# Kernel tuning notes

Hardware: AMD Instinct MI355X
Metric: run time of the kernel (lower is better)

Reference implementation:

```python
import jax, jax.numpy as jnp
import numpy as np
import math

B, S, HID = 2, 2048, 2048
NH, NKV, HD = 16, 4, 128
ROPE_BASE = 10000.0

def _rope(x, position_ids):
    # x: [B, H, S, HD], position_ids: [B, S]
    half = HD // 2
    inv_freq = 1.0 / (ROPE_BASE ** (jnp.arange(0, half, dtype=jnp.float32) / half))
    freqs = position_ids.astype(jnp.float32)[:, :, None] * inv_freq[None, None, :]  # [B,S,half]
    cos = jnp.cos(freqs)[:, None, :, :]  # [B,1,S,half]
    sin = jnp.sin(freqs)[:, None, :, :]
    x1, x2 = x[..., :half], x[..., half:]
    return jnp.concatenate([x1 * cos - x2 * sin, x2 * cos + x1 * sin], axis=-1)

def setup_inputs() -> dict:
    key = jax.random.key(0)
    k1, k2, k3 = jax.random.split(key, 3)
    x = jax.random.normal(k1, (B, S, HID), dtype=jnp.float32)
    position_ids = jnp.broadcast_to(jnp.arange(S, dtype=jnp.int64 if jax.config.jax_enable_x64 else jnp.int32)[None, :], (B, S))
    causal = jnp.tril(jnp.ones((S, S), dtype=bool))
    mask = jnp.where(causal, 0.0, -1e9).astype(jnp.float32)[None, None, :, :]
    w_qkv = jax.random.normal(k2, (NH * HD + 2 * NKV * HD, HID), dtype=jnp.float32) * 0.02
    w_o = jax.random.normal(k3, (HID, HID), dtype=jnp.float32) * 0.02
    return {"x": x, "position_ids": position_ids, "mask": mask, "w_qkv": w_qkv, "w_o": w_o}

def reference(x, position_ids, mask, w_qkv, w_o):
    qkv = x @ w_qkv.T  # [B,S,3072]
    q_dim, kv_dim = NH * HD, NKV * HD
    q = qkv[..., :q_dim].reshape(B, S, NH, HD).transpose(0, 2, 1, 3)          # [B,NH,S,HD]
    k = qkv[..., q_dim:q_dim + kv_dim].reshape(B, S, NKV, HD).transpose(0, 2, 1, 3)
    v = qkv[..., q_dim + kv_dim:].reshape(B, S, NKV, HD).transpose(0, 2, 1, 3)
    q = _rope(q, position_ids)
    k = _rope(k, position_ids)
    n_rep = NH // NKV
    k = jnp.repeat(k, n_rep, axis=1)  # [B,NH,S,HD]
    v = jnp.repeat(v, n_rep, axis=1)
    scores = jnp.einsum('bhqd,bhkd->bhqk', q, k) / math.sqrt(HD) + mask
    attn = jax.nn.softmax(scores, axis=-1)  # dropout p=0.0 -> identity
    out = jnp.einsum('bhqk,bhkd->bhqd', attn, v)
    out = out.transpose(0, 2, 1, 3).reshape(B, S, HID)
    return out @ w_o.T
```

## Files before the change

### kernel.cpp

```cpp
#include <hip/hip_runtime.h>
#include <hip/hip_bf16.h>
#include <cstdint>
#include <cstddef>

typedef unsigned short u16;
typedef __attribute__((ext_vector_type(8))) __bf16 bf16x8;
typedef __attribute__((ext_vector_type(4))) float floatx4;

#define B_    2
#define S_    2048
#define HID_  2048
#define NH_   16
#define NKV_  4
#define HD_   128
#define QKVN_ 3072

__device__ __forceinline__ float bf2f(u16 u) {
  union { unsigned int i; float f; } v; v.i = ((unsigned int)u) << 16; return v.f;
}
__device__ __forceinline__ u16 f2bf(float f) {
  union { float f; unsigned int i; } v; v.f = f;
  unsigned int u = v.i;
  return (u16)((u + 0x7fffu + ((u >> 16) & 1u)) >> 16);
}

#define GLOAD_LDS16(gp, lp)                                                  \
  __builtin_amdgcn_global_load_lds(                                          \
      (__attribute__((address_space(1))) void*)(gp),                         \
      (__attribute__((address_space(3))) void*)(lp), 16, 0, 0)

__global__ __launch_bounds__(256)
void cast_f32_bf16(const float* __restrict__ in, u16* __restrict__ out, int n)
{
  const int i = (blockIdx.x * 256 + threadIdx.x) * 8;
  if (i >= n) return;
  const float4 a = *(const float4*)(in + i);
  const float4 b = *(const float4*)(in + i + 4);
  union { u16 h[8]; uint4 v; } o;
  o.h[0] = f2bf(a.x); o.h[1] = f2bf(a.y); o.h[2] = f2bf(a.z); o.h[3] = f2bf(a.w);
  o.h[4] = f2bf(b.x); o.h[5] = f2bf(b.y); o.h[6] = f2bf(b.z); o.h[7] = f2bf(b.w);
  *(uint4*)(out + i) = o.v;
}

template <bool F32OUT>
__global__ __launch_bounds__(256, 2)
void gemm_bt_128(const u16* __restrict__ A, const u16* __restrict__ W,
                 void* __restrict__ Cv, int N, int K, int lda, int ldc)
{
  __shared__ __align__(16) u16 lA[128 * 64];
  __shared__ __align__(16) u16 lB[128 * 64];
  const int tid  = threadIdx.x;
  const int w    = tid >> 6, ln = tid & 63;
  const int quad = ln >> 4,  l15 = ln & 15;
  const int m0 = blockIdx.y * 128, n0 = blockIdx.x * 128;
  const int waveM = (w >> 1) * 64, waveN = (w & 1) * 64;

  const floatx4 vzero = {0.f, 0.f, 0.f, 0.f};
  floatx4 acc[4][4];
#pragma unroll
  for (int i = 0; i < 4; ++i)
#pragma unroll
    for (int j = 0; j < 4; ++j) acc[i][j] = vzero;

  for (int k0 = 0; k0 < K; k0 += 64) {
    __syncthreads();
#pragma unroll
    for (int p = 0; p < 4; ++p) {
      const int L = (p * 4 + w) * 64 + ln;
      const int row = L >> 3, c = L & 7;
      GLOAD_LDS16(A + (size_t)(m0 + row) * lda + k0 + c * 8, lA + L * 8);
      GLOAD_LDS16(W + (size_t)(n0 + row) * K   + k0 + c * 8, lB + L * 8);
    }
    __syncthreads();
#pragma unroll
    for (int kk = 0; kk < 64; kk += 32) {
      bf16x8 aF[4], bF[4];
      const int cbase = (kk >> 3) + quad;
#pragma unroll
      for (int t = 0; t < 4; ++t) {
        const int rowA = waveM + t * 16 + l15;
        aF[t] = *(const bf16x8*)(lA + rowA * 64 + cbase * 8);
        const int rowB = waveN + t * 16 + l15;
        bF[t] = *(const bf16x8*)(lB + rowB * 64 + cbase * 8);
      }
#pragma unroll
      for (int i = 0; i < 4; ++i)
#pragma unroll
        for (int j = 0; j < 4; ++j)
          acc[i][j] = __builtin_amdgcn_mfma_f32_16x16x32_bf16(aF[i], bF[j], acc[i][j], 0, 0, 0);
    }
  }
#pragma unroll
  for (int i = 0; i < 4; ++i)
#pragma unroll
    for (int r = 0; r < 4; ++r) {
      const int row = m0 + waveM + i * 16 + quad * 4 + r;
      if (F32OUT) {
        float* cp = (float*)Cv + (size_t)row * ldc + n0 + waveN + l15;
#pragma unroll
        for (int j = 0; j < 4; ++j) cp[j * 16] = acc[i][j][r];
      } else {
        u16* cp = (u16*)Cv + (size_t)row * ldc + n0 + waveN + l15;
#pragma unroll
        for (int j = 0; j < 4; ++j) cp[j * 16] = f2bf(acc[i][j][r]);
      }
    }
}

__global__ __launch_bounds__(256)
void rope_inplace(u16* __restrict__ qkv, u16* __restrict__ vt_ws)
{
  const int s = blockIdx.x, b = blockIdx.y;
  const int tid = threadIdx.x;
  __shared__ float cs[64], sn[64];
  if (tid < 64) {
    const float inv = powf(10000.0f, -((float)tid) / 64.0f);
    float s_, c_;
    sincosf((float)s * inv, &s_, &c_);
    cs[tid] = c_; sn[tid] = s_;
  }
  __syncthreads();
  u16* base = qkv + ((size_t)b * S_ + s) * QKVN_;
  for (int p = tid; p < NH_ * 64; p += 256) {
    const int h = p >> 6, i = p & 63;
    u16* hp = base + h * 128;
    const float x1 = bf2f(hp[i]);
    const float x2 = bf2f(hp[64 + i]);
    hp[i]      = f2bf(x1 * cs[i] - x2 * sn[i]);
    hp[64 + i] = f2bf(x2 * cs[i] + x1 * sn[i]);
  }
  for (int p = tid; p < NKV_ * 64; p += 256) {
    const int h = p >> 6, i = p & 63;
    u16* hp = base + NH_ * HD_ + h * 128;
    const float x1 = bf2f(hp[i]);
    const float x2 = bf2f(hp[64 + i]);
    hp[i]      = f2bf(x1 * cs[i] - x2 * sn[i]);
    hp[64 + i] = f2bf(x2 * cs[i] + x1 * sn[i]);
  }
  for (int p = tid; p < NKV_ * HD_; p += 256) {
    const int h = p >> 7, d = p & 127;
    vt_ws[((size_t)(b * NKV_ + h) * HD_ + d) * S_ + s] =
        base[NH_ * HD_ + NKV_ * HD_ + h * 128 + d];
  }
}

#define LPP 68
#define KSLOT(key, s) ((key) * 128 + (((s) ^ ((key) & 7)) * 8))
#define VSLOT(d, s)   ((d) * 64  + (((s) ^ ((d) & 7)) * 8))

__global__ __launch_bounds__(256, 2)
void flash_attn(u16* __restrict__ qkv, const u16* __restrict__ vt_ws)
{
  const int qt = 31 - (int)blockIdx.x;
  const int h  = blockIdx.y;
  const int b  = blockIdx.z;
  const int tid  = threadIdx.x;
  const int w    = tid >> 6, ln = tid & 63;
  const int quad = ln >> 4,  l15 = ln & 15;
  const int kvh  = h >> 2;

  __shared__ __align__(16) u16 lK[2][64 * 128];
  __shared__ __align__(16) u16 lVt[2][128 * 64];
  __shared__ __align__(16) u16 lP[4][16 * LPP];

  const float scale = 0.08838834764831845f;
  const u16* kbase = qkv + (size_t)b * S_ * QKVN_ + NH_ * HD_ + kvh * HD_;
  const u16* vbase = vt_ws + (size_t)(b * NKV_ + kvh) * HD_ * S_;
  const floatx4 vzero = {0.f, 0.f, 0.f, 0.f};

  const int qrow0 = qt * 64 + w * 16;

  bf16x8 qF[4];
  {
    const u16* qp = qkv + ((size_t)(b * S_) + qrow0 + l15) * QKVN_ + h * HD_;
#pragma unroll
    for (int c = 0; c < 4; ++c)
      qF[c] = *(const bf16x8*)(qp + c * 32 + quad * 8);
  }

  float m_i[4], l_i[4];
  floatx4 Oacc[8];
#pragma unroll
  for (int r = 0; r < 4; ++r) { m_i[r] = -1e30f; l_i[r] = 0.f; }
#pragma unroll
  for (int t = 0; t < 8; ++t) Oacc[t] = vzero;

#pragma unroll
  for (int p = 0; p < 4; ++p) {
    const int idx = (w * 4 + p) * 64 + ln;
    const int key = idx >> 4, ks = idx & 15;
    GLOAD_LDS16(kbase + (size_t)key * QKVN_ + ((ks ^ (key & 7)) * 8),
                lK[0] + (w * 4 + p) * 512);
    const int d = idx >> 3, vs = idx & 7;
    GLOAD_LDS16(vbase + (size_t)d * S_ + ((vs ^ (d & 7)) * 8),
                lVt[0] + (w * 4 + p) * 512);
  }

  const int ktEnd = qt + 1;
#pragma unroll 1
  for (int kt = 0; kt < ktEnd; ++kt) {
    const u16* lKc = lK[kt & 1];
    const u16* lVc = lVt[kt & 1];
    const bool pf = (kt + 1 < ktEnd);
    if (pf) {
      u16* lKn = lK[(kt + 1) & 1];
      u16* lVn = lVt[(kt + 1) & 1];
#pragma unroll
      for (int p = 0; p < 4; ++p) {
        const int idx = (w * 4 + p) * 64 + ln;
        const int key = idx >> 4, ks = idx & 15;
        GLOAD_LDS16(kbase + (size_t)((kt + 1) * 64 + key) * QKVN_ + ((ks ^ (key & 7)) * 8),
                    lKn + (w * 4 + p) * 512);
        const int d = idx >> 3, vs = idx & 7;
        GLOAD_LDS16(vbase + (size_t)d * S_ + (kt + 1) * 64 + ((vs ^ (d & 7)) * 8),
                    lVn + (w * 4 + p) * 512);
      }
      asm volatile("s_waitcnt vmcnt(8)" ::: "memory");
    } else {
      asm volatile("s_waitcnt vmcnt(0)" ::: "memory");
    }
    __builtin_amdgcn_s_barrier();
    __builtin_amdgcn_sched_barrier(0);

    floatx4 sc[4];
#pragma unroll
    for (int nt = 0; nt < 4; ++nt) {
      floatx4 a = vzero;
      const int keyloc = nt * 16 + l15;
#pragma unroll
      for (int c = 0; c < 4; ++c) {
        const bf16x8 kF = *(const bf16x8*)(lKc + KSLOT(keyloc, c * 4 + quad));
        a = __builtin_amdgcn_mfma_f32_16x16x32_bf16(qF[c], kF, a, 0, 0, 0);
      }
      sc[nt] = a;
    }

    float pr[4][4];
#pragma unroll
    for (int r = 0; r < 4; ++r) {
      const int qrow = qrow0 + quad * 4 + r;
      float s[4];
#pragma unroll
      for (int nt = 0; nt < 4; ++nt) {
        const int key0 = kt * 64 + nt * 16 + l15;
        s[nt] = sc[nt][r] * scale + ((key0 <= qrow) ? 0.f : -1e9f);
      }
      float mx = fmaxf(fmaxf(s[0], s[1]), fmaxf(s[2], s[3]));
#pragma unroll
      for (int off = 1; off < 16; off <<= 1) mx = fmaxf(mx, __shfl_xor(mx, off, 64));
      const float mn = fmaxf(m_i[r], mx);
      const float alpha = __expf(m_i[r] - mn);
      float sm = 0.f;
#pragma unroll
      for (int nt = 0; nt < 4; ++nt) {
        const float p = __expf(s[nt] - mn);
        pr[nt][r] = p;
        sm += p;
      }
#pragma unroll
      for (int off = 1; off < 16; off <<= 1) sm += __shfl_xor(sm, off, 64);
      l_i[r] = l_i[r] * alpha + sm;
      m_i[r] = mn;
#pragma unroll
      for (int t = 0; t < 8; ++t) Oacc[t][r] *= alpha;
    }

#pragma unroll
    for (int nt = 0; nt < 4; ++nt)
#pragma unroll
      for (int r = 0; r < 4; ++r)
        lP[w][(quad * 4 + r) * LPP + nt * 16 + l15] = f2bf(pr[nt][r]);

    {
      const bf16x8 pF0 = *(const bf16x8*)(&lP[w][l15 * LPP + quad * 8]);
      const bf16x8 pF1 = *(const bf16x8*)(&lP[w][l15 * LPP + 32 + quad * 8]);
#pragma unroll
      for (int t = 0; t < 8; ++t) {
        const int d = t * 16 + l15;
        const bf16x8 vF0 = *(const bf16x8*)(lVc + VSLOT(d, quad));
        const bf16x8 vF1 = *(const bf16x8*)(lVc + VSLOT(d, 4 + quad));
        Oacc[t] = __builtin_amdgcn_mfma_f32_16x16x32_bf16(pF0, vF0, Oacc[t], 0, 0, 0);
        Oacc[t] = __builtin_amdgcn_mfma_f32_16x16x32_bf16(pF1, vF1, Oacc[t], 0, 0, 0);
      }
    }

    __builtin_amdgcn_s_barrier();
  }

#pragma unroll
  for (int r = 0; r < 4; ++r) l_i[r] = 1.0f / l_i[r];
#pragma unroll
  for (int t = 0; t < 8; ++t) {
    const int d = t * 16 + l15;
#pragma unroll
    for (int r = 0; r < 4; ++r) {
      const int qrow = qrow0 + quad * 4 + r;
      qkv[((size_t)(b * S_ + qrow)) * QKVN_ + h * HD_ + d] = f2bf(Oacc[t][r] * l_i[r]);
    }
  }
}

extern "C" void kernel_launch(void* const* d_in, const int* in_sizes, int n_in,
                              void* d_out, int out_size, void* d_ws, size_t ws_size,
                              hipStream_t stream)
{
  (void)in_sizes; (void)n_in; (void)out_size; (void)ws_size;
  const float* x     = (const float*)d_in[0];
  const float* w_qkv = (const float*)d_in[3];
  const float* w_o   = (const float*)d_in[4];
  float* out = (float*)d_out;

  const int nX  = B_ * S_ * HID_;
  const int nWq = QKVN_ * HID_;
  const int nWo = HID_ * HID_;

  u16* ws    = (u16*)d_ws;
  u16* qkv   = ws;
  u16* slotW = qkv + (size_t)(B_ * S_) * QKVN_;
  u16* xb    = (u16*)d_out;
  u16* vt_ws = (u16*)d_out;

  const dim3 blk(256);
  cast_f32_bf16<<<nX  / 2048, blk, 0, stream>>>(x,     xb,    nX);
  cast_f32_bf16<<<nWq / 2048, blk, 0, stream>>>(w_qkv, slotW, nWq);
  gemm_bt_128<false><<<dim3(QKVN_ / 128, (B_ * S_) / 128), blk, 0, stream>>>(
      xb, slotW, qkv, QKVN_, HID_, HID_, QKVN_);
  rope_inplace<<<dim3(S_, B_), blk, 0, stream>>>(qkv, vt_ws);
  cast_f32_bf16<<<nWo / 2048, blk, 0, stream>>>(w_o, slotW, nWo);
  flash_attn<<<dim3(32, NH_, B_), blk, 0, stream>>>(qkv, vt_ws);
  gemm_bt_128<true><<<dim3(HID_ / 128, (B_ * S_) / 128), blk, 0, stream>>>(
      qkv, slotW, out, HID_, HID_, QKVN_, HID_);
}
```

Measured before the change: 420.3 us.

## Pair causal query tiles per block to balance flash attention work

Each flash-attention block now handles two query tiles, a long one (31-pi) and a short one (pi), running 33 KV iterations in one continuous double-buffered loop. The grid halves from 32 to 16 tiles per head, so every block does equal work. This removes the load imbalance of causal attention and the tail it causes. It costs extra registers for the second Q fragment and leaves fewer blocks (512) to fill 256 CUs at 2 blocks per CU.

```diff
diff --git a/kernel.cpp b/kernel.cpp
--- a/kernel.cpp
+++ b/kernel.cpp
@@ -151,7 +151,7 @@
 __global__ __launch_bounds__(256, 2)
 void flash_attn(u16* __restrict__ qkv, const u16* __restrict__ vt_ws)
 {
-  const int qt = 31 - (int)blockIdx.x;
+  const int pi = blockIdx.x;
   const int h  = blockIdx.y;
   const int b  = blockIdx.z;
   const int tid  = threadIdx.x;
@@ -159,6 +159,10 @@
   const int quad = ln >> 4,  l15 = ln & 15;
   const int kvh  = h >> 2;
 
+  const int qtA = 31 - pi, qtB = pi;
+  const int itA = qtA + 1;
+  const int nIt = itA + qtB + 1;
+
   __shared__ __align__(16) u16 lK[2][64 * 128];
   __shared__ __align__(16) u16 lVt[2][128 * 64];
   __shared__ __align__(16) u16 lP[4][16 * LPP];
@@ -168,14 +172,15 @@
   const u16* vbase = vt_ws + (size_t)(b * NKV_ + kvh) * HD_ * S_;
   const floatx4 vzero = {0.f, 0.f, 0.f, 0.f};
 
-  const int qrow0 = qt * 64 + w * 16;
-
-  bf16x8 qF[4];
+  bf16x8 qFA[4], qFB[4];
   {
-    const u16* qp = qkv + ((size_t)(b * S_) + qrow0 + l15) * QKVN_ + h * HD_;
-#pragma unroll
-    for (int c = 0; c < 4; ++c)
-      qF[c] = *(const bf16x8*)(qp + c * 32 + quad * 8);
+    const u16* qpA = qkv + ((size_t)(b * S_) + qtA * 64 + w * 16 + l15) * QKVN_ + h * HD_;
+    const u16* qpB = qkv + ((size_t)(b * S_) + qtB * 64 + w * 16 + l15) * QKVN_ + h * HD_;
+#pragma unroll
+    for (int c = 0; c < 4; ++c) {
+      qFA[c] = *(const bf16x8*)(qpA + c * 32 + quad * 8);
+      qFB[c] = *(const bf16x8*)(qpB + c * 32 + quad * 8);
+    }
   }
 
   float m_i[4], l_i[4];
@@ -184,6 +189,12 @@
   for (int r = 0; r < 4; ++r) { m_i[r] = -1e30f; l_i[r] = 0.f; }
 #pragma unroll
   for (int t = 0; t < 8; ++t) Oacc[t] = vzero;
+
+  bf16x8 qF[4];
+#pragma unroll
+  for (int c = 0; c < 4; ++c) qF[c] = qFA[c];
+  int qtC = qtA;
+  int qrow0 = qtA * 64 + w * 16;
 
 #pragma unroll
   for (int p = 0; p < 4; ++p) {
@@ -196,23 +207,24 @@
                 lVt[0] + (w * 4 + p) * 512);
   }
 
-  const int ktEnd = qt + 1;
 #pragma unroll 1
-  for (int kt = 0; kt < ktEnd; ++kt) {
-    const u16* lKc = lK[kt & 1];
-    const u16* lVc = lVt[kt & 1];
-    const bool pf = (kt + 1 < ktEnd);
+  for (int it = 0; it < nIt; ++it) {
+    const int ktC = (it < itA) ? it : (it - itA);
+    const u16* lKc = lK[it & 1];
+    const u16* lVc = lVt[it & 1];
+    const bool pf = (it + 1 < nIt);
     if (pf) {
-      u16* lKn = lK[(kt + 1) & 1];
-      u16* lVn = lVt[(kt + 1) & 1];
+      const int ktN = (it + 1 < itA) ? (it + 1) : (it + 1 - itA);
+      u16* lKn = lK[(it + 1) & 1];
+      u16* lVn = lVt[(it + 1) & 1];
 #pragma unroll
       for (int p = 0; p < 4; ++p) {
         const int idx = (w * 4 + p) * 64 + ln;
         const int key = idx >> 4, ks = idx & 15;
-        GLOAD_LDS16(kbase + (size_t)((kt + 1) * 64 + key) * QKVN_ + ((ks ^ (key & 7)) * 8),
+        GLOAD_LDS16(kbase + (size_t)(ktN * 64 + key) * QKVN_ + ((ks ^ (key & 7)) * 8),
                     lKn + (w * 4 + p) * 512);
         const int d = idx >> 3, vs = idx & 7;
-        GLOAD_LDS16(vbase + (size_t)d * S_ + (kt + 1) * 64 + ((vs ^ (d & 7)) * 8),
+        GLOAD_LDS16(vbase + (size_t)d * S_ + ktN * 64 + ((vs ^ (d & 7)) * 8),
                     lVn + (w * 4 + p) * 512);
       }
       asm volatile("s_waitcnt vmcnt(8)" ::: "memory");
@@ -242,7 +254,7 @@
       float s[4];
 #pragma unroll
       for (int nt = 0; nt < 4; ++nt) {
-        const int key0 = kt * 64 + nt * 16 + l15;
+        const int key0 = ktC * 64 + nt * 16 + l15;
         s[nt] = sc[nt][r] * scale + ((key0 <= qrow) ? 0.f : -1e9f);
       }
       float mx = fmaxf(fmaxf(s[0], s[1]), fmaxf(s[2], s[3]));
@@ -284,19 +296,33 @@
       }
     }
 
+    if (ktC == qtC) {
+      float linv[4];
+#pragma unroll
+      for (int r = 0; r < 4; ++r) linv[r] = 1.0f / l_i[r];
+#pragma unroll
+      for (int t = 0; t < 8; ++t) {
+        const int d = t * 16 + l15;
+#pragma unroll
+        for (int r = 0; r < 4; ++r) {
+          const int qrow = qrow0 + quad * 4 + r;
+          qkv[((size_t)(b * S_ + qrow)) * QKVN_ + h * HD_ + d] =
+              f2bf(Oacc[t][r] * linv[r]);
+        }
+      }
+      if (pf) {
+        qtC = qtB;
+        qrow0 = qtB * 64 + w * 16;
+#pragma unroll
+        for (int c = 0; c < 4; ++c) qF[c] = qFB[c];
+#pragma unroll
+        for (int r = 0; r < 4; ++r) { m_i[r] = -1e30f; l_i[r] = 0.f; }
+#pragma unroll
+        for (int t = 0; t < 8; ++t) Oacc[t] = vzero;
+      }
+    }
+
     __builtin_amdgcn_s_barrier();
-  }
-
-#pragma unroll
-  for (int r = 0; r < 4; ++r) l_i[r] = 1.0f / l_i[r];
-#pragma unroll
-  for (int t = 0; t < 8; ++t) {
-    const int d = t * 16 + l15;
-#pragma unroll
-    for (int r = 0; r < 4; ++r) {
-      const int qrow = qrow0 + quad * 4 + r;
-      qkv[((size_t)(b * S_ + qrow)) * QKVN_ + h * HD_ + d] = f2bf(Oacc[t][r] * l_i[r]);
-    }
   }
 }
 
@@ -327,7 +353,7 @@
       xb, slotW, qkv, QKVN_, HID_, HID_, QKVN_);
   rope_inplace<<<dim3(S_, B_), blk, 0, stream>>>(qkv, vt_ws);
   cast_f32_bf16<<<nWo / 2048, blk, 0, stream>>>(w_o, slotW, nWo);
-  flash_attn<<<dim3(32, NH_, B_), blk, 0, stream>>>(qkv, vt_ws);
+  flash_attn<<<dim3(16, NH_, B_), blk, 0, stream>>>(qkv, vt_ws);
   gemm_bt_128<true><<<dim3(HID_ / 128, (B_ * S_) / 128), blk, 0, stream>>>(
       qkv, slotW, out, HID_, HID_, QKVN_, HID_);
 }
```

New measurement: 346.8 us. 17.5% less time.
